# Performance work log

Hardware: AMD Instinct MI355X
Metric: run time of the kernel (lower is better)

Reference implementation:

```python
import jax, jax.numpy as jnp
import numpy as np

V, J, NB, NP = 100000, 24, 10, 207
PARENT = np.array([-1, 0, 0, 0, 1, 2, 3, 4, 5, 6, 7, 8, 9, 9, 9, 12, 13, 14, 16, 17, 18, 19, 20, 21])


def setup_inputs() -> dict:
    key = jax.random.key(0)
    ks = jax.random.split(key, 9)
    return {
        "beta": jax.random.normal(ks[0], (NB,), jnp.float32),
        "pose": jax.random.normal(ks[1], (J, 3), jnp.float32),
        "trans": jax.random.normal(ks[2], (3,), jnp.float32),
        "shapedirs": jax.random.normal(ks[3], (V, 3, NB), jnp.float32),
        "v_template": jax.random.normal(ks[4], (V, 3), jnp.float32),
        "J_regressor": jax.random.uniform(ks[5], (J, V), jnp.float32),
        "posedirs": jax.random.normal(ks[6], (V, 3, NP), jnp.float32),
        "weights": jax.random.uniform(ks[7], (V, J), jnp.float32),
        "faces": jax.random.randint(ks[8], (200000, 3), 0, V, jnp.int32),
    }


def _rodrigues(r):
    # r: [N,3] axis-angle -> [N,3,3] rotation matrices
    theta = jnp.sqrt(jnp.sum(r * r, axis=1, keepdims=True)) + 1e-8  # [N,1]
    rh = r / theta
    c = jnp.cos(theta)[:, :, None]  # [N,1,1]
    s = jnp.sin(theta)[:, :, None]
    z = jnp.zeros_like(rh[:, 0])
    K = jnp.stack([z, -rh[:, 2], rh[:, 1],
                   rh[:, 2], z, -rh[:, 0],
                   -rh[:, 1], rh[:, 0], z], axis=1).reshape(-1, 3, 3)
    outer = rh[:, :, None] * rh[:, None, :]
    I = jnp.eye(3, dtype=r.dtype)
    return c * I + (1.0 - c) * outer + s * K


def _with_zeros(Rt):
    # [3,4] -> [4,4] homogeneous
    bottom = jnp.array([[0.0, 0.0, 0.0, 1.0]], dtype=Rt.dtype)
    return jnp.concatenate([Rt, bottom], axis=0)


def reference(beta, pose, trans, shapedirs, v_template, J_regressor, posedirs, weights, faces):
    # shape blending
    v_shaped = jnp.einsum('vdb,b->vd', shapedirs, beta) + v_template  # [V,3]
    Jts = J_regressor @ v_shaped  # [J,3]
    R = _rodrigues(pose)  # [J,3,3]
    # pose blending: lrotmin = (R[1:] - I).flatten(), length 207
    lrotmin = (R[1:] - jnp.eye(3, dtype=R.dtype)).reshape(-1)
    v_posed = v_shaped + jnp.einsum('vdp,p->vd', posedirs, lrotmin)
    # forward kinematics along the 24-joint chain
    G = [_with_zeros(jnp.concatenate([R[0], Jts[0][:, None]], axis=1))]
    for i in range(1, J):
        p = int(PARENT[i])
        loc = _with_zeros(jnp.concatenate([R[i], (Jts[i] - Jts[p])[:, None]], axis=1))
        G.append(G[p] @ loc)
    stacked = jnp.stack(G, axis=0)  # [J,4,4]
    Jh = jnp.concatenate([Jts, jnp.zeros((J, 1), dtype=Jts.dtype)], axis=1)  # [J,4]
    corr = stacked @ Jh[:, :, None]  # [J,4,1]
    A = stacked - jnp.concatenate([jnp.zeros((J, 4, 3), dtype=stacked.dtype), corr], axis=2)
    # LBS skinning
    T = jnp.einsum('vj,jab->vab', weights, A)  # [V,4,4]
    rest = jnp.concatenate([v_posed, jnp.ones((v_posed.shape[0], 1), dtype=v_posed.dtype)], axis=1)  # [V,4]
    v = jnp.einsum('vab,vb->va', T, rest)[:, :3]
    vertices = v + trans[None, :]
    return vertices, faces
```

## Files before the change

### kernel.cpp

```cpp
#include <hip/hip_runtime.h>

#define V_N 100000
#define J_N 24
#define NB_N 10
#define NP_N 207
#define FLAT_P 621
#define FACE_I 600000
#define CHUNKS 50
#define CHUNK_V 2000

__device__ __constant__ int PARENT_D[24] = {
    -1, 0, 0, 0, 1, 2, 3, 4, 5, 6, 7, 8, 9, 9, 9, 12, 13, 14, 16, 17, 18, 19, 20, 21
};

__device__ __forceinline__ float wave_sum64(float x) {
    float t;
    t = __int_as_float(__builtin_amdgcn_update_dpp(0, __float_as_int(x), 0x111, 0xf, 0xf, true)); x += t;
    t = __int_as_float(__builtin_amdgcn_update_dpp(0, __float_as_int(x), 0x112, 0xf, 0xf, true)); x += t;
    t = __int_as_float(__builtin_amdgcn_update_dpp(0, __float_as_int(x), 0x114, 0xf, 0xf, true)); x += t;
    t = __int_as_float(__builtin_amdgcn_update_dpp(0, __float_as_int(x), 0x118, 0xf, 0xf, true)); x += t;
    t = __int_as_float(__builtin_amdgcn_update_dpp(0, __float_as_int(x), 0x142, 0xa, 0xf, true)); x += t;
    t = __int_as_float(__builtin_amdgcn_update_dpp(0, __float_as_int(x), 0x143, 0xc, 0xf, true)); x += t;
    return __int_as_float(__builtin_amdgcn_readlane(__float_as_int(x), 63));
}

__global__ __launch_bounds__(256) void k1_shape(const float* __restrict__ shapedirs,
                                                const float* __restrict__ vtemp,
                                                const float* __restrict__ beta,
                                                float* __restrict__ vshaped) {
    int i = blockIdx.x * 256 + threadIdx.x;
    if (i >= V_N * 3) return;
    const float2* sd2 = reinterpret_cast<const float2*>(shapedirs + (size_t)i * NB_N);
    float2 p0 = sd2[0], p1 = sd2[1], p2 = sd2[2], p3 = sd2[3], p4 = sd2[4];
    float acc = vtemp[i];
    acc += p0.x * beta[0] + p0.y * beta[1];
    acc += p1.x * beta[2] + p1.y * beta[3];
    acc += p2.x * beta[4] + p2.y * beta[5];
    acc += p3.x * beta[6] + p3.y * beta[7];
    acc += p4.x * beta[8] + p4.y * beta[9];
    vshaped[i] = acc;
}

__global__ __launch_bounds__(256) void k2a_partial(const float* __restrict__ Jreg,
                                                   const float* __restrict__ vshaped,
                                                   float* __restrict__ partials) {
    int c = blockIdx.x, j = blockIdx.y;
    int t = threadIdx.x;
    const float* row = Jreg + (size_t)j * V_N + (size_t)c * CHUNK_V;
    const float* vs  = vshaped + (size_t)c * CHUNK_V * 3;
    float s0 = 0.f, s1 = 0.f, s2 = 0.f;
    for (int i = t; i < CHUNK_V; i += 256) {
        float w = row[i];
        s0 += w * vs[i * 3 + 0];
        s1 += w * vs[i * 3 + 1];
        s2 += w * vs[i * 3 + 2];
    }
    for (int off = 32; off > 0; off >>= 1) {
        s0 += __shfl_xor(s0, off, 64);
        s1 += __shfl_xor(s1, off, 64);
        s2 += __shfl_xor(s2, off, 64);
    }
    __shared__ float ls[3][4];
    int wv = t >> 6;
    if ((t & 63) == 0) { ls[0][wv] = s0; ls[1][wv] = s1; ls[2][wv] = s2; }
    __syncthreads();
    if (t == 0) {
        float* p = partials + ((size_t)j * CHUNKS + c) * 3;
        p[0] = ls[0][0] + ls[0][1] + ls[0][2] + ls[0][3];
        p[1] = ls[1][0] + ls[1][1] + ls[1][2] + ls[1][3];
        p[2] = ls[2][0] + ls[2][1] + ls[2][2] + ls[2][3];
    }
}

__global__ __launch_bounds__(128) void k2b_reduce(const float* __restrict__ partials,
                                                  float* __restrict__ jts) {
    int u = threadIdx.x;
    if (u < 72) {
        int j = u / 3, d = u % 3;
        float s = 0.f;
        for (int c = 0; c < CHUNKS; ++c) s += partials[((size_t)j * CHUNKS + c) * 3 + d];
        jts[u] = s;
    }
}

__global__ __launch_bounds__(64) void k3_fk(const float* __restrict__ pose,
                                            const float* __restrict__ jts_in,
                                            float* __restrict__ ws_lrot,
                                            float* __restrict__ ws_A) {
    __shared__ float R[24][9];
    __shared__ float G[24][12];
    __shared__ float Jts[24][3];
    int t = threadIdx.x;
    for (int u = t; u < 72; u += 64) (&Jts[0][0])[u] = jts_in[u];
    if (t < 24) {
        float x = pose[t * 3 + 0], y = pose[t * 3 + 1], z = pose[t * 3 + 2];
        float th = sqrtf(x * x + y * y + z * z) + 1e-8f;
        float inv = 1.0f / th;
        float rx = x * inv, ry = y * inv, rz = z * inv;
        float c = cosf(th), s = sinf(th), ic = 1.0f - c;
        R[t][0] = c + ic * rx * rx;      R[t][1] = ic * rx * ry - s * rz;  R[t][2] = ic * rx * rz + s * ry;
        R[t][3] = ic * ry * rx + s * rz; R[t][4] = c + ic * ry * ry;       R[t][5] = ic * ry * rz - s * rx;
        R[t][6] = ic * rz * rx - s * ry; R[t][7] = ic * rz * ry + s * rx;  R[t][8] = c + ic * rz * rz;
    }
    __syncthreads();
    for (int f = t; f < 640; f += 64) {
        float val = 0.0f;
        if (f < FLAT_P) {
            int p = f % NP_N;
            int j = 1 + p / 9;
            int e = p % 9;
            val = R[j][e] - ((e == 0 || e == 4 || e == 8) ? 1.0f : 0.0f);
        }
        ws_lrot[f] = val;
    }
    if (t < 12) {
        int r = t >> 2, c = t & 3;
        G[0][t] = (c < 3) ? R[0][r * 3 + c] : Jts[0][r];
    }
    __syncthreads();
    for (int i = 1; i < J_N; ++i) {
        int p = PARENT_D[i];
        if (t < 12) {
            int r = t >> 2, c = t & 3;
            float sum = (c == 3) ? G[p][r * 4 + 3] : 0.0f;
            #pragma unroll
            for (int k = 0; k < 3; ++k) {
                float loc = (c < 3) ? R[i][k * 3 + c] : (Jts[i][k] - Jts[p][k]);
                sum += G[p][r * 4 + k] * loc;
            }
            G[i][t] = sum;
        }
        __syncthreads();
    }
    for (int u = t; u < 72; u += 64) {
        int j = u / 3, r = u % 3;
        float g0 = G[j][r * 4 + 0], g1 = G[j][r * 4 + 1], g2 = G[j][r * 4 + 2], g3 = G[j][r * 4 + 3];
        float corr = g0 * Jts[j][0] + g1 * Jts[j][1] + g2 * Jts[j][2];
        ws_A[j * 12 + r * 4 + 0] = g0;
        ws_A[j * 12 + r * 4 + 1] = g1;
        ws_A[j * 12 + r * 4 + 2] = g2;
        ws_A[j * 12 + r * 4 + 3] = g3 - corr;
    }
}

__global__ __launch_bounds__(256) void k4_main(const float* __restrict__ posedirs,
                                               const float* __restrict__ weights,
                                               const float* __restrict__ vshaped,
                                               const float* __restrict__ ws_lrot,
                                               const float* __restrict__ ws_A,
                                               const float* __restrict__ trans,
                                               float* __restrict__ out) {
    __shared__ float sL[640];
    __shared__ float sA[288];
    int tid = threadIdx.x;
    for (int i = tid; i < 640; i += 256) sL[i] = ws_lrot[i];
    for (int i = tid; i < 288; i += 256) sA[i] = ws_A[i];
    __syncthreads();

    int lane = tid & 63;
    int v = blockIdx.x * 4 + (tid >> 6);
    if (v >= V_N) return;

    const float* pd = posedirs + (size_t)v * FLAT_P;
    float a0 = 0.f, a1 = 0.f, a2 = 0.f;
    #pragma unroll
    for (int k = 0; k < 10; ++k) {
        int f = lane + k * 64;
        if (f < FLAT_P) {
            float val = pd[f] * sL[f];
            if (f < 207)      a0 += val;
            else if (f < 414) a1 += val;
            else              a2 += val;
        }
    }
    float vp0 = wave_sum64(a0) + vshaped[v * 3 + 0];
    float vp1 = wave_sum64(a1) + vshaped[v * 3 + 1];
    float vp2 = wave_sum64(a2) + vshaped[v * 3 + 2];

    float r0 = 0.f, r1 = 0.f, r2 = 0.f;
    if (lane < J_N) {
        float w = weights[(size_t)v * J_N + lane];
        const float* A = &sA[lane * 12];
        r0 = w * (A[0] * vp0 + A[1] * vp1 + A[2]  * vp2 + A[3]);
        r1 = w * (A[4] * vp0 + A[5] * vp1 + A[6]  * vp2 + A[7]);
        r2 = w * (A[8] * vp0 + A[9] * vp1 + A[10] * vp2 + A[11]);
    }
    float s0 = wave_sum64(r0);
    float s1 = wave_sum64(r1);
    float s2 = wave_sum64(r2);

    if (lane < 3) {
        float res = (lane == 0) ? s0 : (lane == 1) ? s1 : s2;
        out[v * 3 + lane] = res + trans[lane];
    }
}

__global__ __launch_bounds__(256) void k5_faces(const int4* __restrict__ src,
                                                float4* __restrict__ dst, int n4) {
    int i = blockIdx.x * 256 + threadIdx.x;
    if (i < n4) {
        int4 f = src[i];
        dst[i] = make_float4((float)f.x, (float)f.y, (float)f.z, (float)f.w);
    }
}

extern "C" void kernel_launch(void* const* d_in, const int* in_sizes, int n_in,
                              void* d_out, int out_size, void* d_ws, size_t ws_size,
                              hipStream_t stream) {
    const float* beta      = (const float*)d_in[0];
    const float* pose      = (const float*)d_in[1];
    const float* trans     = (const float*)d_in[2];
    const float* shapedirs = (const float*)d_in[3];
    const float* v_template= (const float*)d_in[4];
    const float* J_reg     = (const float*)d_in[5];
    const float* posedirs  = (const float*)d_in[6];
    const float* weights   = (const float*)d_in[7];
    const int*   faces     = (const int*)d_in[8];

    float* out = (float*)d_out;

    float* ws       = (float*)d_ws;
    float* vshaped  = ws;
    float* jts      = ws + 300000;
    float* ws_lrot  = ws + 300080;
    float* ws_A     = ws + 300720;
    float* partials = ws + 301008;

    k1_shape<<<(V_N * 3 + 255) / 256, 256, 0, stream>>>(shapedirs, v_template, beta, vshaped);
    k2a_partial<<<dim3(CHUNKS, J_N), 256, 0, stream>>>(J_reg, vshaped, partials);
    k2b_reduce<<<1, 128, 0, stream>>>(partials, jts);
    k3_fk<<<1, 64, 0, stream>>>(pose, jts, ws_lrot, ws_A);
    k4_main<<<(V_N + 3) / 4, 256, 0, stream>>>(posedirs, weights, vshaped, ws_lrot, ws_A, trans, out);

    k5_faces<<<(FACE_I / 4 + 255) / 256, 256, 0, stream>>>((const int4*)faces,
                                                            (float4*)(out + 300000), FACE_I / 4);
}
```

Baseline: 90.68 us.

## Merge faces conversion into shape kernel and fold joint reduce into FK

The face index int-to-float conversion now runs as extra blocks of the shape-blend kernel instead of as a separate launch. The partial joint sums are reduced inside the single-block forward-kinematics kernel rather than in their own tiny kernel. Together this cuts the pipeline from six launches to four and removes two launch gaps. The catch is that the FK kernel now does the 50-term serial reduction itself, and the faces work now runs before the joint chain instead of after it.

```diff
diff --git a/kernel.cpp b/kernel.cpp
--- a/kernel.cpp
+++ b/kernel.cpp
@@ -8,6 +8,8 @@
 #define FACE_I 600000
 #define CHUNKS 50
 #define CHUNK_V 2000
+#define K1_BLK 1172
+#define F_BLK  587
 
 __device__ __constant__ int PARENT_D[24] = {
     -1, 0, 0, 0, 1, 2, 3, 4, 5, 6, 7, 8, 9, 9, 9, 12, 13, 14, 16, 17, 18, 19, 20, 21
@@ -24,26 +26,38 @@
     return __int_as_float(__builtin_amdgcn_readlane(__float_as_int(x), 63));
 }
 
-__global__ __launch_bounds__(256) void k1_shape(const float* __restrict__ shapedirs,
-                                                const float* __restrict__ vtemp,
-                                                const float* __restrict__ beta,
-                                                float* __restrict__ vshaped) {
-    int i = blockIdx.x * 256 + threadIdx.x;
-    if (i >= V_N * 3) return;
-    const float2* sd2 = reinterpret_cast<const float2*>(shapedirs + (size_t)i * NB_N);
-    float2 p0 = sd2[0], p1 = sd2[1], p2 = sd2[2], p3 = sd2[3], p4 = sd2[4];
-    float acc = vtemp[i];
-    acc += p0.x * beta[0] + p0.y * beta[1];
-    acc += p1.x * beta[2] + p1.y * beta[3];
-    acc += p2.x * beta[4] + p2.y * beta[5];
-    acc += p3.x * beta[6] + p3.y * beta[7];
-    acc += p4.x * beta[8] + p4.y * beta[9];
-    vshaped[i] = acc;
-}
-
-__global__ __launch_bounds__(256) void k2a_partial(const float* __restrict__ Jreg,
-                                                   const float* __restrict__ vshaped,
-                                                   float* __restrict__ partials) {
+__global__ __launch_bounds__(256) void kA_shape_faces(const float* __restrict__ shapedirs,
+                                                      const float* __restrict__ vtemp,
+                                                      const float* __restrict__ beta,
+                                                      float* __restrict__ vshaped,
+                                                      const int4* __restrict__ faces4,
+                                                      float* __restrict__ out) {
+    int b = blockIdx.x;
+    if (b < K1_BLK) {
+        int i = b * 256 + threadIdx.x;
+        if (i >= V_N * 3) return;
+        const float2* sd2 = reinterpret_cast<const float2*>(shapedirs + (size_t)i * NB_N);
+        float2 p0 = sd2[0], p1 = sd2[1], p2 = sd2[2], p3 = sd2[3], p4 = sd2[4];
+        float acc = vtemp[i];
+        acc += p0.x * beta[0] + p0.y * beta[1];
+        acc += p1.x * beta[2] + p1.y * beta[3];
+        acc += p2.x * beta[4] + p2.y * beta[5];
+        acc += p3.x * beta[6] + p3.y * beta[7];
+        acc += p4.x * beta[8] + p4.y * beta[9];
+        vshaped[i] = acc;
+    } else {
+        int i = (b - K1_BLK) * 256 + threadIdx.x;
+        if (i < FACE_I / 4) {
+            int4 f = faces4[i];
+            float4* fdst = reinterpret_cast<float4*>(out + 300000);
+            fdst[i] = make_float4((float)f.x, (float)f.y, (float)f.z, (float)f.w);
+        }
+    }
+}
+
+__global__ __launch_bounds__(256) void kB_partial(const float* __restrict__ Jreg,
+                                                  const float* __restrict__ vshaped,
+                                                  float* __restrict__ partials) {
     int c = blockIdx.x, j = blockIdx.y;
     int t = threadIdx.x;
     const float* row = Jreg + (size_t)j * V_N + (size_t)c * CHUNK_V;
@@ -72,26 +86,20 @@
     }
 }
 
-__global__ __launch_bounds__(128) void k2b_reduce(const float* __restrict__ partials,
-                                                  float* __restrict__ jts) {
-    int u = threadIdx.x;
-    if (u < 72) {
-        int j = u / 3, d = u % 3;
-        float s = 0.f;
-        for (int c = 0; c < CHUNKS; ++c) s += partials[((size_t)j * CHUNKS + c) * 3 + d];
-        jts[u] = s;
-    }
-}
-
-__global__ __launch_bounds__(64) void k3_fk(const float* __restrict__ pose,
-                                            const float* __restrict__ jts_in,
+__global__ __launch_bounds__(64) void kC_fk(const float* __restrict__ pose,
+                                            const float* __restrict__ partials,
                                             float* __restrict__ ws_lrot,
                                             float* __restrict__ ws_A) {
     __shared__ float R[24][9];
     __shared__ float G[24][12];
     __shared__ float Jts[24][3];
     int t = threadIdx.x;
-    for (int u = t; u < 72; u += 64) (&Jts[0][0])[u] = jts_in[u];
+    for (int u = t; u < 72; u += 64) {
+        int j = u / 3, d = u % 3;
+        float s = 0.f;
+        for (int c = 0; c < CHUNKS; ++c) s += partials[((size_t)j * CHUNKS + c) * 3 + d];
+        (&Jts[0][0])[u] = s;
+    }
     if (t < 24) {
         float x = pose[t * 3 + 0], y = pose[t * 3 + 1], z = pose[t * 3 + 2];
         float th = sqrtf(x * x + y * y + z * z) + 1e-8f;
@@ -143,7 +151,7 @@
     }
 }
 
-__global__ __launch_bounds__(256) void k4_main(const float* __restrict__ posedirs,
+__global__ __launch_bounds__(256) void kD_main(const float* __restrict__ posedirs,
                                                const float* __restrict__ weights,
                                                const float* __restrict__ vshaped,
                                                const float* __restrict__ ws_lrot,
@@ -192,15 +200,6 @@
     if (lane < 3) {
         float res = (lane == 0) ? s0 : (lane == 1) ? s1 : s2;
         out[v * 3 + lane] = res + trans[lane];
-    }
-}
-
-__global__ __launch_bounds__(256) void k5_faces(const int4* __restrict__ src,
-                                                float4* __restrict__ dst, int n4) {
-    int i = blockIdx.x * 256 + threadIdx.x;
-    if (i < n4) {
-        int4 f = src[i];
-        dst[i] = make_float4((float)f.x, (float)f.y, (float)f.z, (float)f.w);
     }
 }
 
@@ -221,17 +220,13 @@
 
     float* ws       = (float*)d_ws;
     float* vshaped  = ws;
-    float* jts      = ws + 300000;
     float* ws_lrot  = ws + 300080;
     float* ws_A     = ws + 300720;
     float* partials = ws + 301008;
 
-    k1_shape<<<(V_N * 3 + 255) / 256, 256, 0, stream>>>(shapedirs, v_template, beta, vshaped);
-    k2a_partial<<<dim3(CHUNKS, J_N), 256, 0, stream>>>(J_reg, vshaped, partials);
-    k2b_reduce<<<1, 128, 0, stream>>>(partials, jts);
-    k3_fk<<<1, 64, 0, stream>>>(pose, jts, ws_lrot, ws_A);
-    k4_main<<<(V_N + 3) / 4, 256, 0, stream>>>(posedirs, weights, vshaped, ws_lrot, ws_A, trans, out);
-
-    k5_faces<<<(FACE_I / 4 + 255) / 256, 256, 0, stream>>>((const int4*)faces,
-                                                            (float4*)(out + 300000), FACE_I / 4);
-}
+    kA_shape_faces<<<K1_BLK + F_BLK, 256, 0, stream>>>(shapedirs, v_template, beta, vshaped,
+                                                       (const int4*)faces, out);
+    kB_partial<<<dim3(CHUNKS, J_N), 256, 0, stream>>>(J_reg, vshaped, partials);
+    kC_fk<<<1, 64, 0, stream>>>(pose, partials, ws_lrot, ws_A);
+    kD_main<<<(V_N + 3) / 4, 256, 0, stream>>>(posedirs, weights, vshaped, ws_lrot, ws_A, trans, out);
+}
```

New measurement: 89.24 us. No clear change (-1.6%).
